# Kernel tuning notes

Hardware: AMD Instinct MI355X
Metric: run time of the kernel (lower is better)

## Reference

```python
import jax, jax.numpy as jnp
import numpy as np

N = 20000
E = 600000
D = 512
H = 8
HD = D // H
HID = 1024
FIN = D + 3 * H  # forces_mlp input dim = 536
SCALE = 1.0 / float(np.sqrt(HD))


def _ln(x, g, b, eps=1e-5):
    m = x.mean(-1, keepdims=True)
    v = x.var(-1, keepdims=True)
    return (x - m) / jnp.sqrt(v + eps) * g + b


def _resmlp(h, Wi, bi, Wh, bh, Wo, bo):
    # ResMLP with layers=3: in-proj, one residual hidden block, out-proj
    h = jax.nn.gelu(h @ Wi + bi)
    h = h + jax.nn.gelu(h @ Wh + bh)
    return h @ Wo + bo


def setup_inputs() -> dict:
    key = jax.random.key(0)
    ks = jax.random.split(key, 24)
    s = 0.02
    x = jax.random.normal(ks[0], (N, D), jnp.float32)
    edge_index = jax.random.randint(ks[1], (2, E), 0, N, dtype=jnp.int32)
    att_bias = jax.random.normal(ks[2], (E,), jnp.float32)
    pos = jax.random.normal(ks[3], (N, 3), jnp.float32)
    batch = jnp.zeros((N,), jnp.int32)
    return {
        "x": x, "edge_index": edge_index, "att_bias": att_bias, "pos": pos, "batch": batch,
        "g_att": jnp.ones((D,), jnp.float32), "b_att": jnp.zeros((D,), jnp.float32),
        "g_mlp": jnp.ones((D,), jnp.float32), "b_mlp": jnp.zeros((D,), jnp.float32),
        "Wq": jax.random.normal(ks[4], (D, D), jnp.float32) * s, "bq": jnp.zeros((D,), jnp.float32),
        "Wk": jax.random.normal(ks[5], (D, D), jnp.float32) * s, "bk": jnp.zeros((D,), jnp.float32),
        "We_in": jax.random.normal(ks[6], (D, HID), jnp.float32) * s, "be_in": jnp.zeros((HID,), jnp.float32),
        "We_h": jax.random.normal(ks[7], (HID, HID), jnp.float32) * s, "be_h": jnp.zeros((HID,), jnp.float32),
        "We_out": jax.random.normal(ks[8], (HID, 1), jnp.float32) * s, "be_out": jnp.zeros((1,), jnp.float32),
        "Wf_in": jax.random.normal(ks[9], (FIN, HID), jnp.float32) * s, "bf_in": jnp.zeros((HID,), jnp.float32),
        "Wf_h": jax.random.normal(ks[10], (HID, HID), jnp.float32) * s, "bf_h": jnp.zeros((HID,), jnp.float32),
        "Wf_out": jax.random.normal(ks[11], (HID, 3), jnp.float32) * s, "bf_out": jnp.zeros((3,), jnp.float32),
    }


def reference(x, edge_index, att_bias, pos, batch,
              g_att, b_att, g_mlp, b_mlp, Wq, bq, Wk, bk,
              We_in, be_in, We_h, be_h, We_out, be_out,
              Wf_in, bf_in, Wf_h, bf_h, Wf_out, bf_out):
    n = x.shape[0]
    row, col = edge_index[0], edge_index[1]

    z_att = _ln(x, g_att, b_att)
    q = (z_att @ Wq + bq).reshape(n, H, HD)  # [N,H,HD]
    k = (z_att @ Wk + bk).reshape(n, H, HD)

    # sparse scaled dot product restricted to edges, with additive per-edge bias
    logits = jnp.einsum('ehd,ehd->eh', q[row], k[col]) * SCALE + att_bias[:, None]  # [E,H]
    mx = jax.ops.segment_max(logits, row, num_segments=n)          # [N,H]
    mx = jnp.where(jnp.isfinite(mx), mx, 0.0)
    p = jnp.exp(logits - mx[row])
    denom = jax.ops.segment_sum(p, row, num_segments=n)            # [N,H]
    w = p / denom[row]                                             # [E,H]

    contrib = jnp.einsum('eh,ec->ehc', w, pos[col])                # [E,H,3]
    att = jax.ops.segment_sum(contrib, row, num_segments=n)        # [N,H,3]
    att = att - pos[:, None, :]                                    # att - value
    att = att.reshape(n, H * 3)                                    # permute(1,0,2).view(N,-1)

    z_mlp = _ln(x, g_mlp, b_mlp)
    energy = _resmlp(z_mlp, We_in, be_in, We_h, be_h, We_out, be_out)
    forces = _resmlp(jnp.concatenate([z_mlp, att], axis=-1), Wf_in, bf_in, Wf_h, bf_h, Wf_out, bf_out)
    return (energy, forces)
```

## Files before the change

### kernel.cpp

```cpp
#include <hip/hip_runtime.h>

#define NN 20000
#define EE 600000

typedef unsigned short u16;
typedef unsigned int u32;
typedef float f32x4 __attribute__((ext_vector_type(4)));
typedef u32 u32x4 __attribute__((ext_vector_type(4)));

__device__ __forceinline__ u16 f2bf(float f){
  u32 u = __float_as_uint(f);
  return (u16)((u + 0x7fffu + ((u>>16)&1u))>>16);
}
__device__ __forceinline__ float bf2f(u16 h){ return __uint_as_float(((u32)h)<<16); }

__device__ __forceinline__ float gelu_f(float x){
  float u = 0.7978845608028654f*(x + 0.044715f*x*x*x);
  float e = __expf(2.0f*u);
  return 0.5f*x*(2.0f - 2.0f/(e+1.0f));
}

__global__ __launch_bounds__(256) void ln2_kernel(
    const float* __restrict__ x,
    const float* __restrict__ ga, const float* __restrict__ ba,
    const float* __restrict__ gm, const float* __restrict__ bm,
    u16* __restrict__ za, u16* __restrict__ xf, int N)
{
  int row = (blockIdx.x<<2) + (threadIdx.x>>6);
  int lane = threadIdx.x & 63;
  if(row >= N) return;
  const float* xp = x + ((size_t)row<<9) + (lane<<3);
  f32x4 v0 = *(const f32x4*)xp;
  f32x4 v1 = *(const f32x4*)(xp+4);
  float vals[8] = {v0[0],v0[1],v0[2],v0[3],v1[0],v1[1],v1[2],v1[3]};
  float s=0.f, qs=0.f;
#pragma unroll
  for(int i=0;i<8;i++){ s += vals[i]; qs = fmaf(vals[i],vals[i],qs); }
#pragma unroll
  for(int o=1;o<64;o<<=1){ s += __shfl_xor(s,o); qs += __shfl_xor(qs,o); }
  float mean = s*(1.f/512.f);
  float var  = qs*(1.f/512.f) - mean*mean;
  float rstd = rsqrtf(var + 1e-5f);
  int c0 = lane<<3;
#pragma unroll
  for(int i=0;i<8;i++){
    float zn = (vals[i]-mean)*rstd;
    za[((size_t)row<<9)+c0+i]  = f2bf(fmaf(zn, ga[c0+i], ba[c0+i]));
    xf[(size_t)row*576+c0+i]   = f2bf(fmaf(zn, gm[c0+i], bm[c0+i]));
  }
}

__global__ __launch_bounds__(256) void wtt_kernel(
    const float* __restrict__ W, u16* __restrict__ WT, int K, int Nn, int Kpad)
{
  __shared__ u16 tile[64][65];
  const int k0 = blockIdx.x<<6, n0 = blockIdx.y<<6;
  const int tx = threadIdx.x & 63, ty = threadIdx.x >> 6;
#pragma unroll
  for(int i=0;i<16;i++){
    int r = (i<<2) + ty;
    int gk = k0 + r;
    float v = (gk < K) ? W[(size_t)gk*Nn + n0 + tx] : 0.f;
    tile[r][tx] = f2bf(v);
  }
  __syncthreads();
#pragma unroll
  for(int i=0;i<16;i++){
    int r = (i<<2) + ty;
    WT[(size_t)(n0 + r)*Kpad + k0 + tx] = tile[tx][r];
  }
}

__global__ __launch_bounds__(256) void gemm_bt(
    const u16* __restrict__ A, const u16* __restrict__ B,
    const float* __restrict__ bias, const u16* __restrict__ resid,
    u16* __restrict__ Cb, const float* __restrict__ wout,
    float* __restrict__ outp,
    int M, int N, int K, int lda, int ldr, int mode)
{
  __shared__ u16 As[128*64];
  __shared__ u16 Bs[128*64];
  const int gx = gridDim.x;
  const int b  = blockIdx.y*gx + blockIdx.x;
  const int xcd = b & 7, loc = b >> 3;
  const int tileM = ((loc/gx)*8 + xcd) << 7;
  const int tileN = (loc % gx) << 7;
  if(tileM >= M) return;
  const int tid  = threadIdx.x;
  const int wave = tid>>6, lane = tid&63;
  const int quad = lane>>4, l15 = lane&15;
  const int mhalf = (wave>>1)<<6, nhalf = (wave&1)<<6;
  f32x4 acc[4][4] = {};

  for(int k0=0; k0<K; k0+=64){
#pragma unroll
    for(int j=0;j<4;j++){
      const int c   = (((wave<<2)+j)<<6) + lane;
      const int row = c>>3;
      const int cc  = (c&7) ^ (row&7);
      int gr = tileM + row; gr = (gr < M) ? gr : (M-1);
      const u16* gp = A + (size_t)gr*lda + (size_t)(k0 + (cc<<3));
      __builtin_amdgcn_global_load_lds(
        (const __attribute__((address_space(1))) u32*)gp,
        (__attribute__((address_space(3))) u32*)(&As[((wave<<2)+j)<<9]),
        16, 0, 0);
    }
#pragma unroll
    for(int j=0;j<4;j++){
      const int c   = (((wave<<2)+j)<<6) + lane;
      const int row = c>>3;
      const int cc  = (c&7) ^ (row&7);
      const u16* gp = B + (size_t)(tileN + row)*K + (size_t)(k0 + (cc<<3));
      __builtin_amdgcn_global_load_lds(
        (const __attribute__((address_space(1))) u32*)gp,
        (__attribute__((address_space(3))) u32*)(&Bs[((wave<<2)+j)<<9]),
        16, 0, 0);
    }
    __syncthreads();
#pragma unroll
    for(int ks=0;ks<2;ks++){
      const int ccol = (ks<<2) + quad;
      u32x4 af[4], bfr[4];
#pragma unroll
      for(int mi=0;mi<4;mi++){
        const int row = mhalf + (mi<<4) + l15;
        af[mi] = *(const u32x4*)&As[((row<<3) + (ccol ^ (row&7)))<<3];
      }
#pragma unroll
      for(int ni=0;ni<4;ni++){
        const int row = nhalf + (ni<<4) + l15;
        bfr[ni] = *(const u32x4*)&Bs[((row<<3) + (ccol ^ (row&7)))<<3];
      }
#pragma unroll
      for(int mi=0;mi<4;mi++)
#pragma unroll
        for(int ni=0;ni<4;ni++)
          asm("v_mfma_f32_16x16x32_bf16 %0, %1, %2, %0"
              : "+v"(acc[mi][ni]) : "v"(af[mi]), "v"(bfr[ni]));
    }
    __syncthreads();
  }

  if(mode <= 1){
#pragma unroll
    for(int mi=0;mi<4;mi++){
#pragma unroll
      for(int reg=0;reg<4;reg++){
        const int gr = tileM + mhalf + (mi<<4) + (quad<<2) + reg;
        if(gr < M){
#pragma unroll
          for(int ni=0;ni<4;ni++){
            const int gc = tileN + nhalf + (ni<<4) + l15;
            float v = acc[mi][ni][reg] + bias[gc];
            if(mode == 1) v = gelu_f(v);
            Cb[(size_t)gr*N + gc] = f2bf(v);
          }
        }
      }
    }
  } else if(mode == 2){
    float wv[4], bv[4];
#pragma unroll
    for(int ni=0;ni<4;ni++){
      int gc = tileN + nhalf + (ni<<4) + l15;
      wv[ni] = wout[gc]; bv[ni] = bias[gc];
    }
#pragma unroll
    for(int mi=0;mi<4;mi++){
#pragma unroll
      for(int reg=0;reg<4;reg++){
        const int gr = tileM + mhalf + (mi<<4) + (quad<<2) + reg;
        if(gr < M){
          float vs = 0.f;
#pragma unroll
          for(int ni=0;ni<4;ni++){
            const int gc = tileN + nhalf + (ni<<4) + l15;
            float v = gelu_f(acc[mi][ni][reg] + bv[ni])
                    + bf2f(resid[(size_t)gr*ldr + gc]);
            vs = fmaf(v, wv[ni], vs);
          }
          vs += __shfl_xor(vs,1); vs += __shfl_xor(vs,2);
          vs += __shfl_xor(vs,4); vs += __shfl_xor(vs,8);
          if(l15 == 0) atomicAdd(&outp[gr], vs);
        }
      }
    }
  } else {
    float wv0[4], wv1[4], wv2[4], bv[4];
#pragma unroll
    for(int ni=0;ni<4;ni++){
      int gc = tileN + nhalf + (ni<<4) + l15;
      wv0[ni] = wout[gc*3+0]; wv1[ni] = wout[gc*3+1]; wv2[ni] = wout[gc*3+2];
      bv[ni] = bias[gc];
    }
#pragma unroll
    for(int mi=0;mi<4;mi++){
#pragma unroll
      for(int reg=0;reg<4;reg++){
        const int gr = tileM + mhalf + (mi<<4) + (quad<<2) + reg;
        if(gr < M){
          float s0=0.f, s1=0.f, s2=0.f;
#pragma unroll
          for(int ni=0;ni<4;ni++){
            const int gc = tileN + nhalf + (ni<<4) + l15;
            float v = gelu_f(acc[mi][ni][reg] + bv[ni])
                    + bf2f(resid[(size_t)gr*ldr + gc]);
            s0 = fmaf(v, wv0[ni], s0);
            s1 = fmaf(v, wv1[ni], s1);
            s2 = fmaf(v, wv2[ni], s2);
          }
          s0 += __shfl_xor(s0,1); s0 += __shfl_xor(s0,2); s0 += __shfl_xor(s0,4); s0 += __shfl_xor(s0,8);
          s1 += __shfl_xor(s1,1); s1 += __shfl_xor(s1,2); s1 += __shfl_xor(s1,4); s1 += __shfl_xor(s1,8);
          s2 += __shfl_xor(s2,1); s2 += __shfl_xor(s2,2); s2 += __shfl_xor(s2,4); s2 += __shfl_xor(s2,8);
          if(l15 == 0){
            atomicAdd(&outp[(size_t)gr*3+0], s0);
            atomicAdd(&outp[(size_t)gr*3+1], s1);
            atomicAdd(&outp[(size_t)gr*3+2], s2);
          }
        }
      }
    }
  }
}

__global__ __launch_bounds__(256) void out_init_kernel(
    float* __restrict__ out, const float* __restrict__ beO,
    const float* __restrict__ bfO)
{
  int idx = blockIdx.x*256 + threadIdx.x;
  if(idx < NN) out[idx] = beO[0];
  else if(idx < NN*4) out[idx] = bfO[(idx - NN) % 3];
}

__global__ __launch_bounds__(256) void hist_kernel(
    const int* __restrict__ ei, int* __restrict__ deg, int E)
{
  int e = blockIdx.x*256 + threadIdx.x;
  if(e < E) atomicAdd(&deg[ei[e]], 1);
}

__global__ __launch_bounds__(1024) void scan_kernel(
    const int* __restrict__ deg, int* __restrict__ rowptr,
    int* __restrict__ cursor, int N)
{
  __shared__ int wsum[16];
  __shared__ int carry_s;
  const int tid = threadIdx.x, lane = tid & 63, wid = tid >> 6;
  if(tid == 0) carry_s = 0;
  __syncthreads();
  for(int base = 0; base < N; base += 1024){
    int idx = base + tid;
    int v = (idx < N) ? deg[idx] : 0;
    int s = v;
#pragma unroll
    for(int o=1;o<64;o<<=1){ int t = __shfl_up(s,o); if(lane>=o) s += t; }
    if(lane==63) wsum[wid] = s;
    __syncthreads();
    if(wid==0 && lane<16){
      int ws = wsum[lane];
      int t = ws;
#pragma unroll
      for(int o=1;o<16;o<<=1){ int u = __shfl_up(t,o); if(lane>=o) t += u; }
      wsum[lane] = t - ws;
    }
    __syncthreads();
    int ex = s - v + wsum[wid] + carry_s;
    if(idx < N){ rowptr[idx] = ex; cursor[idx] = ex; }
    __syncthreads();
    if(tid == 1023) carry_s += wsum[15] + s;
  }
  __syncthreads();
  if(tid == 0) rowptr[N] = carry_s;
}

__global__ __launch_bounds__(256) void scatter_kernel(
    const int* __restrict__ ei, const float* __restrict__ ab,
    int* __restrict__ cursor, int* __restrict__ cols,
    float* __restrict__ abs_, int E)
{
  int e = blockIdx.x*256 + threadIdx.x;
  if(e >= E) return;
  int r = ei[e];
  int p = atomicAdd(&cursor[r], 1);
  cols[p] = ei[EE + e];
  abs_[p] = ab[e];
}

__global__ __launch_bounds__(256) void node_att_kernel(
    const u16* __restrict__ qk, const int* __restrict__ rowptr,
    const int* __restrict__ cols, const float* __restrict__ abs_,
    const float* __restrict__ pos, u16* __restrict__ xf, int N)
{
  const int node = (blockIdx.x<<2) + (threadIdx.x>>6);
  const int lane = threadIdx.x & 63;
  if(node >= N) return;
  const int h = lane>>3, sub = lane&7;
  const u32x4 qv = *(const u32x4*)(qk + ((size_t)node<<10) + (lane<<3));
  const float posn = (sub<3) ? pos[node*3 + sub] : 0.f;
  const int j1 = rowptr[node+1];
  float den = 0.f, nm = 0.f;

  int j = rowptr[node];
  for(; j+3 < j1; j += 4){
    int c[4]; float abv[4], pv[4]; u32x4 kv[4];
#pragma unroll
    for(int t=0;t<4;t++){ c[t] = cols[j+t]; abv[t] = abs_[j+t]; }
#pragma unroll
    for(int t=0;t<4;t++){
      kv[t] = *(const u32x4*)(qk + ((size_t)c[t]<<10) + 512 + (lane<<3));
      pv[t] = (sub<3) ? pos[c[t]*3+sub] : 0.f;
    }
#pragma unroll
    for(int t=0;t<4;t++){
      float s = 0.f;
#pragma unroll
      for(int i=0;i<4;i++){
        s = fmaf(__uint_as_float(qv[i]<<16),         __uint_as_float(kv[t][i]<<16), s);
        s = fmaf(__uint_as_float(qv[i]&0xffff0000u), __uint_as_float(kv[t][i]&0xffff0000u), s);
      }
      s += __shfl_xor(s,1); s += __shfl_xor(s,2); s += __shfl_xor(s,4);
      float p = __expf(fmaf(s, 0.125f, abv[t]));
      den += p;
      nm = fmaf(p, pv[t], nm);
    }
  }
  for(; j < j1; j++){
    int c0 = cols[j];
    u32x4 kv0 = *(const u32x4*)(qk + ((size_t)c0<<10) + 512 + (lane<<3));
    float pv0 = (sub<3) ? pos[c0*3+sub] : 0.f;
    float s0=0.f;
#pragma unroll
    for(int i=0;i<4;i++){
      s0 = fmaf(__uint_as_float(qv[i]<<16),        __uint_as_float(kv0[i]<<16), s0);
      s0 = fmaf(__uint_as_float(qv[i]&0xffff0000u),__uint_as_float(kv0[i]&0xffff0000u), s0);
    }
    s0 += __shfl_xor(s0,1); s0 += __shfl_xor(s0,2); s0 += __shfl_xor(s0,4);
    float p0 = __expf(fmaf(s0, 0.125f, abs_[j]));
    den += p0;
    nm = fmaf(p0, pv0, nm);
  }

  u16* xp = xf + (size_t)node*576;
  if(sub < 3){
    float a = (den > 0.f) ? nm/den : 0.f;
    xp[512 + h*3 + sub] = f2bf(a - posn);
  } else {
    xp[536 + h*5 + (sub-3)] = 0;
  }
}

extern "C" void kernel_launch(void* const* d_in, const int* in_sizes, int n_in,
                              void* d_out, int out_size, void* d_ws, size_t ws_size,
                              hipStream_t stream)
{
  (void)in_sizes; (void)n_in; (void)out_size; (void)ws_size;
  const float* x    = (const float*)d_in[0];
  const int*   ei   = (const int*)d_in[1];
  const float* ab   = (const float*)d_in[2];
  const float* pos  = (const float*)d_in[3];
  const float* g_att= (const float*)d_in[5];
  const float* b_att= (const float*)d_in[6];
  const float* g_mlp= (const float*)d_in[7];
  const float* b_mlp= (const float*)d_in[8];
  const float* Wq   = (const float*)d_in[9];  const float* bq  = (const float*)d_in[10];
  const float* Wk   = (const float*)d_in[11]; const float* bk  = (const float*)d_in[12];
  const float* WeI  = (const float*)d_in[13]; const float* beI = (const float*)d_in[14];
  const float* WeH  = (const float*)d_in[15]; const float* beH = (const float*)d_in[16];
  const float* WeO  = (const float*)d_in[17]; const float* beO = (const float*)d_in[18];
  const float* WfI  = (const float*)d_in[19]; const float* bfI = (const float*)d_in[20];
  const float* WfH  = (const float*)d_in[21]; const float* bfH = (const float*)d_in[22];
  const float* WfO  = (const float*)d_in[23]; const float* bfO = (const float*)d_in[24];

  char* w = (char*)d_ws;
  size_t off = 0;
  auto alloc = [&](size_t bytes) -> void* {
    void* p = w + off; off += (bytes + 255) & ~(size_t)255; return p;
  };
  u16* zatt  = (u16*)alloc((size_t)NN*512*2);
  u16* qk    = (u16*)alloc((size_t)NN*1024*2);
  u16* xf    = (u16*)alloc((size_t)NN*576*2);
  u16* h1cat = (u16*)alloc((size_t)NN*2048*2);
  u16* wqkT  = (u16*)alloc((size_t)1024*512*2);
  u16* wInT  = (u16*)alloc((size_t)2048*576*2);
  u16* weHT  = (u16*)alloc((size_t)1024*1024*2);
  u16* wfHT  = (u16*)alloc((size_t)1024*1024*2);
  float* bqk    = (float*)alloc((size_t)1024*4);
  float* bcat   = (float*)alloc((size_t)2048*4);
  int*   deg    = (int*)alloc((size_t)NN*4);
  int*   rowptr = (int*)alloc((size_t)(NN+1)*4);
  int*   cursor = (int*)alloc((size_t)NN*4);
  int*   cols   = (int*)alloc((size_t)EE*4);
  float* absrt  = (float*)alloc((size_t)EE*4);

  hipMemsetAsync(deg, 0, (size_t)NN*4, stream);
  hipMemcpyAsync(bqk,        bq,  512*4, hipMemcpyDeviceToDevice, stream);
  hipMemcpyAsync(bqk + 512,  bk,  512*4, hipMemcpyDeviceToDevice, stream);
  hipMemcpyAsync(bcat,       beI, 1024*4, hipMemcpyDeviceToDevice, stream);
  hipMemcpyAsync(bcat + 1024,bfI, 1024*4, hipMemcpyDeviceToDevice, stream);

  wtt_kernel<<<dim3(512/64, 512/64),256,0,stream>>>(Wq, wqkT,           512, 512, 512);
  wtt_kernel<<<dim3(512/64, 512/64),256,0,stream>>>(Wk, wqkT + 512*512, 512, 512, 512);
  wtt_kernel<<<dim3(576/64, 1024/64),256,0,stream>>>(WeI, wInT,              512, 1024, 576);
  wtt_kernel<<<dim3(576/64, 1024/64),256,0,stream>>>(WfI, wInT + 1024*576,   536, 1024, 576);
  wtt_kernel<<<dim3(1024/64,1024/64),256,0,stream>>>(WeH, weHT, 1024, 1024, 1024);
  wtt_kernel<<<dim3(1024/64,1024/64),256,0,stream>>>(WfH, wfHT, 1024, 1024, 1024);

  out_init_kernel<<<dim3((NN*4+255)/256),256,0,stream>>>((float*)d_out, beO, bfO);

  ln2_kernel<<<dim3((NN+3)/4),256,0,stream>>>(x, g_att,b_att, g_mlp,b_mlp, zatt, xf, NN);

  hist_kernel   <<<dim3((EE+255)/256),256,0,stream>>>(ei, deg, EE);
  scan_kernel   <<<1,1024,0,stream>>>(deg, rowptr, cursor, NN);
  scatter_kernel<<<dim3((EE+255)/256),256,0,stream>>>(ei, ab, cursor, cols, absrt, EE);

  const int MT = 160;

  gemm_bt<<<dim3(8, MT),256,0,stream>>>(zatt, wqkT, bqk, nullptr, qk,
                                        nullptr, nullptr, NN, 1024, 512, 512, 0, 0);

  node_att_kernel<<<dim3((NN+3)/4),256,0,stream>>>(qk, rowptr, cols, absrt, pos, xf, NN);

  gemm_bt<<<dim3(16, MT),256,0,stream>>>(xf, wInT, bcat, nullptr, h1cat,
                                         nullptr, nullptr, NN, 2048, 576, 576, 0, 1);

  gemm_bt<<<dim3(8, MT),256,0,stream>>>(h1cat, weHT, beH, h1cat, nullptr,
                                        WeO, (float*)d_out,
                                        NN, 1024, 1024, 2048, 2048, 2);
  gemm_bt<<<dim3(8, MT),256,0,stream>>>(h1cat+1024, wfHT, bfH, h1cat+1024, nullptr,
                                        WfO, (float*)d_out + NN,
                                        NN, 1024, 1024, 2048, 2048, 3);
}
```

Measured before the change: 639.0 us.

## Double-buffer GEMM LDS tiles and merge energy/force hidden GEMMs into one launch

The GEMM kernel now double-buffers its A and B tiles in LDS. The next K-slice is issued with global_load_lds while MFMAs run on the current slice, and one barrier per iteration is removed. The two residual hidden-layer GEMMs for the energy and force MLPs are merged into a single launch over a concatenated 2048-wide weight. Each block picks its A column offset, output weights and output slot from its tileN. This doubles LDS use per block, which may lower occupancy, and relies on the async loads being ordered correctly by the single remaining barrier.

```diff
diff --git a/kernel.cpp b/kernel.cpp
--- a/kernel.cpp
+++ b/kernel.cpp
@@ -74,35 +74,37 @@
 __global__ __launch_bounds__(256) void gemm_bt(
     const u16* __restrict__ A, const u16* __restrict__ B,
     const float* __restrict__ bias, const u16* __restrict__ resid,
-    u16* __restrict__ Cb, const float* __restrict__ wout,
-    float* __restrict__ outp,
+    u16* __restrict__ Cb, const float* __restrict__ woutE,
+    const float* __restrict__ woutF, float* __restrict__ outp,
     int M, int N, int K, int lda, int ldr, int mode)
 {
-  __shared__ u16 As[128*64];
-  __shared__ u16 Bs[128*64];
+  __shared__ u16 As[2][128*64];
+  __shared__ u16 Bs[2][128*64];
   const int gx = gridDim.x;
   const int b  = blockIdx.y*gx + blockIdx.x;
   const int xcd = b & 7, loc = b >> 3;
   const int tileM = ((loc/gx)*8 + xcd) << 7;
   const int tileN = (loc % gx) << 7;
   if(tileM >= M) return;
+  const int isF = (mode == 2 && tileN >= 1024) ? 1 : 0;
+  const u16* Ab = A + (isF ? 1024 : 0);
   const int tid  = threadIdx.x;
   const int wave = tid>>6, lane = tid&63;
   const int quad = lane>>4, l15 = lane&15;
   const int mhalf = (wave>>1)<<6, nhalf = (wave&1)<<6;
   f32x4 acc[4][4] = {};
 
-  for(int k0=0; k0<K; k0+=64){
+  auto stage = [&](int k0, int buf){
 #pragma unroll
     for(int j=0;j<4;j++){
       const int c   = (((wave<<2)+j)<<6) + lane;
       const int row = c>>3;
       const int cc  = (c&7) ^ (row&7);
       int gr = tileM + row; gr = (gr < M) ? gr : (M-1);
-      const u16* gp = A + (size_t)gr*lda + (size_t)(k0 + (cc<<3));
+      const u16* gp = Ab + (size_t)gr*lda + (size_t)(k0 + (cc<<3));
       __builtin_amdgcn_global_load_lds(
         (const __attribute__((address_space(1))) u32*)gp,
-        (__attribute__((address_space(3))) u32*)(&As[((wave<<2)+j)<<9]),
+        (__attribute__((address_space(3))) u32*)(&As[buf][((wave<<2)+j)<<9]),
         16, 0, 0);
     }
 #pragma unroll
@@ -113,10 +115,16 @@
       const u16* gp = B + (size_t)(tileN + row)*K + (size_t)(k0 + (cc<<3));
       __builtin_amdgcn_global_load_lds(
         (const __attribute__((address_space(1))) u32*)gp,
-        (__attribute__((address_space(3))) u32*)(&Bs[((wave<<2)+j)<<9]),
+        (__attribute__((address_space(3))) u32*)(&Bs[buf][((wave<<2)+j)<<9]),
         16, 0, 0);
     }
+  };
+
+  stage(0, 0);
+  int cur = 0;
+  for(int k0=0; k0<K; k0+=64){
     __syncthreads();
+    if(k0+64 < K) stage(k0+64, cur^1);
 #pragma unroll
     for(int ks=0;ks<2;ks++){
       const int ccol = (ks<<2) + quad;
@@ -124,12 +132,12 @@
 #pragma unroll
       for(int mi=0;mi<4;mi++){
         const int row = mhalf + (mi<<4) + l15;
-        af[mi] = *(const u32x4*)&As[((row<<3) + (ccol ^ (row&7)))<<3];
+        af[mi] = *(const u32x4*)&As[cur][((row<<3) + (ccol ^ (row&7)))<<3];
       }
 #pragma unroll
       for(int ni=0;ni<4;ni++){
         const int row = nhalf + (ni<<4) + l15;
-        bfr[ni] = *(const u32x4*)&Bs[((row<<3) + (ccol ^ (row&7)))<<3];
+        bfr[ni] = *(const u32x4*)&Bs[cur][((row<<3) + (ccol ^ (row&7)))<<3];
       }
 #pragma unroll
       for(int mi=0;mi<4;mi++)
@@ -138,7 +146,7 @@
           asm("v_mfma_f32_16x16x32_bf16 %0, %1, %2, %0"
               : "+v"(acc[mi][ni]) : "v"(af[mi]), "v"(bfr[ni]));
     }
-    __syncthreads();
+    cur ^= 1;
   }
 
   if(mode <= 1){
@@ -158,12 +166,12 @@
         }
       }
     }
-  } else if(mode == 2){
+  } else if(!isF){
     float wv[4], bv[4];
 #pragma unroll
     for(int ni=0;ni<4;ni++){
       int gc = tileN + nhalf + (ni<<4) + l15;
-      wv[ni] = wout[gc]; bv[ni] = bias[gc];
+      wv[ni] = woutE[gc]; bv[ni] = bias[gc];
     }
 #pragma unroll
     for(int mi=0;mi<4;mi++){
@@ -190,7 +198,8 @@
 #pragma unroll
     for(int ni=0;ni<4;ni++){
       int gc = tileN + nhalf + (ni<<4) + l15;
-      wv0[ni] = wout[gc*3+0]; wv1[ni] = wout[gc*3+1]; wv2[ni] = wout[gc*3+2];
+      int wc = gc - 1024;
+      wv0[ni] = woutF[wc*3+0]; wv1[ni] = woutF[wc*3+1]; wv2[ni] = woutF[wc*3+2];
       bv[ni] = bias[gc];
     }
 #pragma unroll
@@ -213,9 +222,9 @@
           s1 += __shfl_xor(s1,1); s1 += __shfl_xor(s1,2); s1 += __shfl_xor(s1,4); s1 += __shfl_xor(s1,8);
           s2 += __shfl_xor(s2,1); s2 += __shfl_xor(s2,2); s2 += __shfl_xor(s2,4); s2 += __shfl_xor(s2,8);
           if(l15 == 0){
-            atomicAdd(&outp[(size_t)gr*3+0], s0);
-            atomicAdd(&outp[(size_t)gr*3+1], s1);
-            atomicAdd(&outp[(size_t)gr*3+2], s2);
+            atomicAdd(&outp[NN + (size_t)gr*3+0], s0);
+            atomicAdd(&outp[NN + (size_t)gr*3+1], s1);
+            atomicAdd(&outp[NN + (size_t)gr*3+2], s2);
           }
         }
       }
@@ -382,10 +391,10 @@
   u16* h1cat = (u16*)alloc((size_t)NN*2048*2);
   u16* wqkT  = (u16*)alloc((size_t)1024*512*2);
   u16* wInT  = (u16*)alloc((size_t)2048*576*2);
-  u16* weHT  = (u16*)alloc((size_t)1024*1024*2);
-  u16* wfHT  = (u16*)alloc((size_t)1024*1024*2);
+  u16* wHT   = (u16*)alloc((size_t)2048*1024*2);
   float* bqk    = (float*)alloc((size_t)1024*4);
   float* bcat   = (float*)alloc((size_t)2048*4);
+  float* bH     = (float*)alloc((size_t)2048*4);
   int*   deg    = (int*)alloc((size_t)NN*4);
   int*   rowptr = (int*)alloc((size_t)(NN+1)*4);
   int*   cursor = (int*)alloc((size_t)NN*4);
@@ -397,13 +406,15 @@
   hipMemcpyAsync(bqk + 512,  bk,  512*4, hipMemcpyDeviceToDevice, stream);
   hipMemcpyAsync(bcat,       beI, 1024*4, hipMemcpyDeviceToDevice, stream);
   hipMemcpyAsync(bcat + 1024,bfI, 1024*4, hipMemcpyDeviceToDevice, stream);
+  hipMemcpyAsync(bH,         beH, 1024*4, hipMemcpyDeviceToDevice, stream);
+  hipMemcpyAsync(bH + 1024,  bfH, 1024*4, hipMemcpyDeviceToDevice, stream);
 
   wtt_kernel<<<dim3(512/64, 512/64),256,0,stream>>>(Wq, wqkT,           512, 512, 512);
   wtt_kernel<<<dim3(512/64, 512/64),256,0,stream>>>(Wk, wqkT + 512*512, 512, 512, 512);
-  wtt_kernel<<<dim3(576/64, 1024/64),256,0,stream>>>(WeI, wInT,              512, 1024, 576);
-  wtt_kernel<<<dim3(576/64, 1024/64),256,0,stream>>>(WfI, wInT + 1024*576,   536, 1024, 576);
-  wtt_kernel<<<dim3(1024/64,1024/64),256,0,stream>>>(WeH, weHT, 1024, 1024, 1024);
-  wtt_kernel<<<dim3(1024/64,1024/64),256,0,stream>>>(WfH, wfHT, 1024, 1024, 1024);
+  wtt_kernel<<<dim3(576/64, 1024/64),256,0,stream>>>(WeI, wInT,            512, 1024, 576);
+  wtt_kernel<<<dim3(576/64, 1024/64),256,0,stream>>>(WfI, wInT + 1024*576, 536, 1024, 576);
+  wtt_kernel<<<dim3(1024/64,1024/64),256,0,stream>>>(WeH, wHT,             1024, 1024, 1024);
+  wtt_kernel<<<dim3(1024/64,1024/64),256,0,stream>>>(WfH, wHT + 1024*1024, 1024, 1024, 1024);
 
   out_init_kernel<<<dim3((NN*4+255)/256),256,0,stream>>>((float*)d_out, beO, bfO);
 
@@ -416,17 +427,16 @@
   const int MT = 160;
 
   gemm_bt<<<dim3(8, MT),256,0,stream>>>(zatt, wqkT, bqk, nullptr, qk,
-                                        nullptr, nullptr, NN, 1024, 512, 512, 0, 0);
+                                        nullptr, nullptr, nullptr,
+                                        NN, 1024, 512, 512, 0, 0);
 
   node_att_kernel<<<dim3((NN+3)/4),256,0,stream>>>(qk, rowptr, cols, absrt, pos, xf, NN);
 
   gemm_bt<<<dim3(16, MT),256,0,stream>>>(xf, wInT, bcat, nullptr, h1cat,
-                                         nullptr, nullptr, NN, 2048, 576, 576, 0, 1);
-
-  gemm_bt<<<dim3(8, MT),256,0,stream>>>(h1cat, weHT, beH, h1cat, nullptr,
-                                        WeO, (float*)d_out,
-                                        NN, 1024, 1024, 2048, 2048, 2);
-  gemm_bt<<<dim3(8, MT),256,0,stream>>>(h1cat+1024, wfHT, bfH, h1cat+1024, nullptr,
-                                        WfO, (float*)d_out + NN,
-                                        NN, 1024, 1024, 2048, 2048, 3);
-}
+                                         nullptr, nullptr, nullptr,
+                                         NN, 2048, 576, 576, 0, 1);
+
+  gemm_bt<<<dim3(16, MT),256,0,stream>>>(h1cat, wHT, bH, h1cat, nullptr,
+                                         WeO, WfO, (float*)d_out,
+                                         NN, 2048, 1024, 2048, 2048, 2);
+}
```

After: 714.9 us. 11.9% more time.

## Double-buffer GEMM LDS tiles with K=32 steps and unroll edge loop to 8

Applied to the files above, without the earlier changes.

The bf16 GEMM now stages 32-wide K slices into two LDS buffers and prefetches the next slice while running MFMAs on the current one, with one barrier per iteration instead of two. The XOR swizzle on LDS rows is dropped, which may add bank conflicts on the fragment reads. Separately, the per-node attention loop gathers 8 neighbour K rows at a time instead of 4 to keep more memory loads in flight, at the cost of more registers.

```diff
diff --git a/kernel.cpp b/kernel.cpp
--- a/kernel.cpp
+++ b/kernel.cpp
@@ -78,8 +78,8 @@
     float* __restrict__ outp,
     int M, int N, int K, int lda, int ldr, int mode)
 {
-  __shared__ u16 As[128*64];
-  __shared__ u16 Bs[128*64];
+  __shared__ u16 As[2][128*32];
+  __shared__ u16 Bs[2][128*32];
   const int gx = gridDim.x;
   const int b  = blockIdx.y*gx + blockIdx.x;
   const int xcd = b & 7, loc = b >> 3;
@@ -92,53 +92,53 @@
   const int mhalf = (wave>>1)<<6, nhalf = (wave&1)<<6;
   f32x4 acc[4][4] = {};
 
-  for(int k0=0; k0<K; k0+=64){
-#pragma unroll
-    for(int j=0;j<4;j++){
-      const int c   = (((wave<<2)+j)<<6) + lane;
-      const int row = c>>3;
-      const int cc  = (c&7) ^ (row&7);
+  auto stage = [&](int k0, int buf){
+#pragma unroll
+    for(int j=0;j<2;j++){
+      const int c   = (((wave<<1)+j)<<6) + lane;
+      const int row = c>>2, kc = c&3;
       int gr = tileM + row; gr = (gr < M) ? gr : (M-1);
-      const u16* gp = A + (size_t)gr*lda + (size_t)(k0 + (cc<<3));
+      const u16* gp = A + (size_t)gr*lda + (size_t)(k0 + (kc<<3));
       __builtin_amdgcn_global_load_lds(
         (const __attribute__((address_space(1))) u32*)gp,
-        (__attribute__((address_space(3))) u32*)(&As[((wave<<2)+j)<<9]),
+        (__attribute__((address_space(3))) u32*)(&As[buf][((wave<<1)+j)<<9]),
         16, 0, 0);
     }
 #pragma unroll
-    for(int j=0;j<4;j++){
-      const int c   = (((wave<<2)+j)<<6) + lane;
-      const int row = c>>3;
-      const int cc  = (c&7) ^ (row&7);
-      const u16* gp = B + (size_t)(tileN + row)*K + (size_t)(k0 + (cc<<3));
+    for(int j=0;j<2;j++){
+      const int c   = (((wave<<1)+j)<<6) + lane;
+      const int row = c>>2, kc = c&3;
+      const u16* gp = B + (size_t)(tileN + row)*K + (size_t)(k0 + (kc<<3));
       __builtin_amdgcn_global_load_lds(
         (const __attribute__((address_space(1))) u32*)gp,
-        (__attribute__((address_space(3))) u32*)(&Bs[((wave<<2)+j)<<9]),
+        (__attribute__((address_space(3))) u32*)(&Bs[buf][((wave<<1)+j)<<9]),
         16, 0, 0);
     }
+  };
+
+  stage(0, 0);
+  int cur = 0;
+  for(int k0=0; k0<K; k0+=32){
     __syncthreads();
-#pragma unroll
-    for(int ks=0;ks<2;ks++){
-      const int ccol = (ks<<2) + quad;
-      u32x4 af[4], bfr[4];
-#pragma unroll
-      for(int mi=0;mi<4;mi++){
-        const int row = mhalf + (mi<<4) + l15;
-        af[mi] = *(const u32x4*)&As[((row<<3) + (ccol ^ (row&7)))<<3];
-      }
-#pragma unroll
-      for(int ni=0;ni<4;ni++){
-        const int row = nhalf + (ni<<4) + l15;
-        bfr[ni] = *(const u32x4*)&Bs[((row<<3) + (ccol ^ (row&7)))<<3];
-      }
-#pragma unroll
-      for(int mi=0;mi<4;mi++)
-#pragma unroll
-        for(int ni=0;ni<4;ni++)
-          asm("v_mfma_f32_16x16x32_bf16 %0, %1, %2, %0"
-              : "+v"(acc[mi][ni]) : "v"(af[mi]), "v"(bfr[ni]));
-    }
-    __syncthreads();
+    if(k0+32 < K) stage(k0+32, cur^1);
+    u32x4 af[4], bfr[4];
+#pragma unroll
+    for(int mi=0;mi<4;mi++){
+      const int row = mhalf + (mi<<4) + l15;
+      af[mi] = *(const u32x4*)&As[cur][((row<<2) + quad)<<3];
+    }
+#pragma unroll
+    for(int ni=0;ni<4;ni++){
+      const int row = nhalf + (ni<<4) + l15;
+      bfr[ni] = *(const u32x4*)&Bs[cur][((row<<2) + quad)<<3];
+    }
+#pragma unroll
+    for(int mi=0;mi<4;mi++)
+#pragma unroll
+      for(int ni=0;ni<4;ni++)
+        asm("v_mfma_f32_16x16x32_bf16 %0, %1, %2, %0"
+            : "+v"(acc[mi][ni]) : "v"(af[mi]), "v"(bfr[ni]));
+    cur ^= 1;
   }
 
   if(mode <= 1){
@@ -301,17 +301,17 @@
   float den = 0.f, nm = 0.f;
 
   int j = rowptr[node];
-  for(; j+3 < j1; j += 4){
-    int c[4]; float abv[4], pv[4]; u32x4 kv[4];
-#pragma unroll
-    for(int t=0;t<4;t++){ c[t] = cols[j+t]; abv[t] = abs_[j+t]; }
-#pragma unroll
-    for(int t=0;t<4;t++){
+  for(; j+7 < j1; j += 8){
+    int c[8]; float abv[8], pv[8]; u32x4 kv[8];
+#pragma unroll
+    for(int t=0;t<8;t++){ c[t] = cols[j+t]; abv[t] = abs_[j+t]; }
+#pragma unroll
+    for(int t=0;t<8;t++){
       kv[t] = *(const u32x4*)(qk + ((size_t)c[t]<<10) + 512 + (lane<<3));
       pv[t] = (sub<3) ? pos[c[t]*3+sub] : 0.f;
     }
 #pragma unroll
-    for(int t=0;t<4;t++){
+    for(int t=0;t<8;t++){
       float s = 0.f;
 #pragma unroll
       for(int i=0;i<4;i++){
@@ -400,8 +400,8 @@
 
   wtt_kernel<<<dim3(512/64, 512/64),256,0,stream>>>(Wq, wqkT,           512, 512, 512);
   wtt_kernel<<<dim3(512/64, 512/64),256,0,stream>>>(Wk, wqkT + 512*512, 512, 512, 512);
-  wtt_kernel<<<dim3(576/64, 1024/64),256,0,stream>>>(WeI, wInT,              512, 1024, 576);
-  wtt_kernel<<<dim3(576/64, 1024/64),256,0,stream>>>(WfI, wInT + 1024*576,   536, 1024, 576);
+  wtt_kernel<<<dim3(576/64, 1024/64),256,0,stream>>>(WeI, wInT,            512, 1024, 576);
+  wtt_kernel<<<dim3(576/64, 1024/64),256,0,stream>>>(WfI, wInT + 1024*576, 536, 1024, 576);
   wtt_kernel<<<dim3(1024/64,1024/64),256,0,stream>>>(WeH, weHT, 1024, 1024, 1024);
   wtt_kernel<<<dim3(1024/64,1024/64),256,0,stream>>>(WfH, wfHT, 1024, 1024, 1024);
 
```

Measured after the change: 713.4 us. +11.6%, slower.
